# Kernel tuning notes

Hardware: AMD Instinct MI355X
Metric: run time of the kernel (lower is better)

Reference implementation:

```python
import jax, jax.numpy as jnp
import numpy as np

N, IN_CH, HID, HEADS, OUT_CH, E = 50000, 128, 64, 4, 16, 800000
NEG_SLOPE = 0.2


def gatv2_layer(x, Wl, Wr, att, b, src, dst, n_nodes, heads, out_ch, concat):
    # lin_l -> source features, lin_r -> target features (PyG GATv2Conv, share_weights=False)
    xl = (x @ Wl).reshape(n_nodes, heads, out_ch)
    xr = (x @ Wr).reshape(n_nodes, heads, out_ch)
    # per-edge attention logits: att . leaky_relu(x_l[j] + x_r[i])
    e = jax.nn.leaky_relu(xl[src] + xr[dst], NEG_SLOPE)        # [E, H, C]
    logits = jnp.einsum('ehc,hc->eh', e, att)                  # [E, H]
    # softmax over incoming edges per target node
    m = jax.ops.segment_max(logits, dst, num_segments=n_nodes)
    ex = jnp.exp(logits - m[dst])
    denom = jax.ops.segment_sum(ex, dst, num_segments=n_nodes)
    alpha = ex / denom[dst]                                    # [E, H]
    # scatter weighted source messages back to targets
    msg = alpha[:, :, None] * xl[src]                          # [E, H, C]
    out = jax.ops.segment_sum(msg, dst, num_segments=n_nodes)  # [N, H, C]
    out = out.reshape(n_nodes, heads * out_ch) if concat else out.mean(axis=1)
    return out + b


def setup_inputs() -> dict:
    key = jax.random.key(0)
    ks = jax.random.split(key, 10)
    x = jax.random.normal(ks[0], (N, IN_CH), dtype=jnp.float32)
    edge_index = jax.random.randint(ks[1], (2, E), 0, N, dtype=jnp.int64)
    s1 = 1.0 / np.sqrt(IN_CH)
    s2 = 1.0 / np.sqrt(HEADS * HID)
    return {
        'x': x,
        'edge_index': edge_index,
        'W1l': jax.random.normal(ks[2], (IN_CH, HEADS * HID), dtype=jnp.float32) * s1,
        'W1r': jax.random.normal(ks[3], (IN_CH, HEADS * HID), dtype=jnp.float32) * s1,
        'att1': jax.random.normal(ks[4], (HEADS, HID), dtype=jnp.float32) * (1.0 / np.sqrt(HID)),
        'b1': jnp.zeros((HEADS * HID,), dtype=jnp.float32),
        'W2l': jax.random.normal(ks[5], (HEADS * HID, OUT_CH), dtype=jnp.float32) * s2,
        'W2r': jax.random.normal(ks[6], (HEADS * HID, OUT_CH), dtype=jnp.float32) * s2,
        'att2': jax.random.normal(ks[7], (1, OUT_CH), dtype=jnp.float32) * (1.0 / np.sqrt(OUT_CH)),
        'b2': jnp.zeros((OUT_CH,), dtype=jnp.float32),
    }


def reference(x, edge_index, W1l, W1r, att1, b1, W2l, W2r, att2, b2):
    # add self loops (PyG GATv2Conv default add_self_loops=True)
    loops = jnp.arange(N, dtype=edge_index.dtype)
    src = jnp.concatenate([edge_index[0], loops])
    dst = jnp.concatenate([edge_index[1], loops])
    h = gatv2_layer(x, W1l, W1r, att1, b1, src, dst, N, HEADS, HID, True)
    h = jax.nn.elu(h)
    out = gatv2_layer(h, W2l, W2r, att2, b2, src, dst, N, 1, OUT_CH, False)
    return out
```

## Files before the change

kernel.cpp:

```cpp
#include <hip/hip_runtime.h>
#include <hip/hip_bf16.h>
#include <math.h>

#define N_NODES 50000
#define IN_CH   128
#define HID     64
#define HEADS   4
#define OUT_CH  16
#define NE      800000
#define ETOT    (NE + N_NODES)
#define NEG_SLOPE 0.2f

__global__ __launch_bounds__(256) void k_gemm1(const float* __restrict__ x,
        const float* __restrict__ Wl, const float* __restrict__ Wr,
        float* __restrict__ out) {
    __shared__ float xs[64][132];
    __shared__ float ws[128][64];
    int rb = blockIdx.x * 64;
    int cb = blockIdx.y * 64;
    const float* W = (cb < 256) ? Wl : Wr;
    int wc = cb & 255;
    int tid = threadIdx.x;
    for (int i = 0; i < 8; ++i) {
        int idx = i * 256 + tid;
        int r = idx >> 5, c4 = idx & 31;
        float4 v = make_float4(0.f, 0.f, 0.f, 0.f);
        int gr = rb + r;
        if (gr < N_NODES) v = *(const float4*)(x + (size_t)gr * IN_CH + c4 * 4);
        *(float4*)&xs[r][c4 * 4] = v;
    }
    for (int i = 0; i < 8; ++i) {
        int idx = i * 256 + tid;
        int r = idx >> 4, c4 = idx & 15;
        *(float4*)&ws[r][c4 * 4] = *(const float4*)(W + (size_t)r * 256 + wc + c4 * 4);
    }
    __syncthreads();
    int cg = tid & 15, rg = tid >> 4;
    int c0 = cg * 4, r0 = rg * 4;
    float acc[4][4];
    #pragma unroll
    for (int i = 0; i < 4; ++i)
        #pragma unroll
        for (int j = 0; j < 4; ++j) acc[i][j] = 0.f;
    for (int k = 0; k < 128; ++k) {
        float xv[4];
        #pragma unroll
        for (int i = 0; i < 4; ++i) xv[i] = xs[r0 + i][k];
        float4 wv = *(float4*)&ws[k][c0];
        #pragma unroll
        for (int i = 0; i < 4; ++i) {
            acc[i][0] += xv[i] * wv.x;
            acc[i][1] += xv[i] * wv.y;
            acc[i][2] += xv[i] * wv.z;
            acc[i][3] += xv[i] * wv.w;
        }
    }
    #pragma unroll
    for (int i = 0; i < 4; ++i) {
        int gr = rb + r0 + i;
        if (gr < N_NODES) {
            float4 v = make_float4(acc[i][0], acc[i][1], acc[i][2], acc[i][3]);
            *(float4*)(out + (size_t)gr * 512 + cb + c0) = v;
        }
    }
}

__global__ void k_count(const int* __restrict__ ei, int* __restrict__ counts) {
    int e = blockIdx.x * blockDim.x + threadIdx.x;
    if (e >= ETOT) return;
    int dst = (e < NE) ? ei[NE + e] : (e - NE);
    atomicAdd(&counts[dst], 1);
}

__global__ __launch_bounds__(256) void k_scanA(const int* __restrict__ counts,
        int* __restrict__ tmp, int* __restrict__ bsums) {
    __shared__ int lds[256];
    int i = blockIdx.x * 256 + threadIdx.x;
    int v = (i < N_NODES) ? counts[i] : 0;
    lds[threadIdx.x] = v;
    __syncthreads();
    int val = v;
    for (int off = 1; off < 256; off <<= 1) {
        int t = (threadIdx.x >= off) ? lds[threadIdx.x - off] : 0;
        __syncthreads();
        val += t;
        lds[threadIdx.x] = val;
        __syncthreads();
    }
    if (i < N_NODES) tmp[i] = val;
    if (threadIdx.x == 255) bsums[blockIdx.x] = val;
}

__global__ __launch_bounds__(256) void k_scanB(const int* __restrict__ bsums,
        int* __restrict__ boff, int nb) {
    __shared__ int lds[256];
    int tid = threadIdx.x;
    int v = (tid < nb) ? bsums[tid] : 0;
    lds[tid] = v;
    __syncthreads();
    int val = v;
    for (int off = 1; off < 256; off <<= 1) {
        int t = (tid >= off) ? lds[tid - off] : 0;
        __syncthreads();
        val += t;
        lds[tid] = val;
        __syncthreads();
    }
    if (tid < nb) boff[tid] = val - v;
}

__global__ void k_scanC(const int* __restrict__ tmp, const int* __restrict__ counts,
        const int* __restrict__ boff, int* __restrict__ rowptr, int* __restrict__ cursor) {
    int i = blockIdx.x * 256 + threadIdx.x;
    if (i >= N_NODES) return;
    int ex = tmp[i] + boff[blockIdx.x] - counts[i];
    rowptr[i] = ex;
    cursor[i] = ex;
    if (i == N_NODES - 1) rowptr[N_NODES] = ex + counts[i];
}

__global__ void k_fill(const int* __restrict__ ei, int* __restrict__ cursor,
        int* __restrict__ csrc) {
    int e = blockIdx.x * blockDim.x + threadIdx.x;
    if (e >= ETOT) return;
    int src, dst;
    if (e < NE) { src = ei[e]; dst = ei[NE + e]; }
    else        { src = e - NE; dst = src; }
    int pos = atomicAdd(&cursor[dst], 1);
    csrc[pos] = src;
}

__device__ __forceinline__ float edge_logit(float4 xl, float4 xr, float4 av) {
    float4 u;
    u.x = xl.x + xr.x; u.y = xl.y + xr.y; u.z = xl.z + xr.z; u.w = xl.w + xr.w;
    u.x = (u.x > 0.f) ? u.x : u.x * NEG_SLOPE;
    u.y = (u.y > 0.f) ? u.y : u.y * NEG_SLOPE;
    u.z = (u.z > 0.f) ? u.z : u.z * NEG_SLOPE;
    u.w = (u.w > 0.f) ? u.w : u.w * NEG_SLOPE;
    return u.x * av.x + u.y * av.y + u.z * av.z + u.w * av.w;
}

__global__ __launch_bounds__(256) void k_agg1(const float* __restrict__ xlxr,
        const int* __restrict__ rowptr, const int* __restrict__ csrc,
        const float* __restrict__ att, const float* __restrict__ b1,
        float* __restrict__ h) {
    int wave = threadIdx.x >> 6, lane = threadIdx.x & 63;
    int d = blockIdx.x * 4 + wave;
    if (d >= N_NODES) return;
    int hh = lane >> 4, cb = (lane & 15) * 4;
    int co = hh * 64 + cb;
    const float* base_l = xlxr + co;
    float4 xr = *(const float4*)(xlxr + (size_t)d * 512 + 256 + co);
    float4 av = *(const float4*)(att + co);
    float m = -1e30f, s = 0.f;
    float4 acc = make_float4(0.f, 0.f, 0.f, 0.f);
    int e0 = rowptr[d], e1 = rowptr[d + 1];
    int i = e0;
    for (; i + 1 < e1; i += 2) {
        int s0 = csrc[i], s1 = csrc[i + 1];
        float4 x0 = *(const float4*)(base_l + (size_t)s0 * 512);
        float4 x1 = *(const float4*)(base_l + (size_t)s1 * 512);
        float t0 = edge_logit(x0, xr, av);
        float t1 = edge_logit(x1, xr, av);
        t0 += __shfl_xor(t0, 8, 64);  t1 += __shfl_xor(t1, 8, 64);
        t0 += __shfl_xor(t0, 4, 64);  t1 += __shfl_xor(t1, 4, 64);
        t0 += __shfl_xor(t0, 2, 64);  t1 += __shfl_xor(t1, 2, 64);
        t0 += __shfl_xor(t0, 1, 64);  t1 += __shfl_xor(t1, 1, 64);
        {
            float nm = fmaxf(m, t0);
            float sc = __expf(m - nm), p = __expf(t0 - nm);
            s = s * sc + p;
            acc.x = acc.x * sc + p * x0.x;
            acc.y = acc.y * sc + p * x0.y;
            acc.z = acc.z * sc + p * x0.z;
            acc.w = acc.w * sc + p * x0.w;
            m = nm;
        }
        {
            float nm = fmaxf(m, t1);
            float sc = __expf(m - nm), p = __expf(t1 - nm);
            s = s * sc + p;
            acc.x = acc.x * sc + p * x1.x;
            acc.y = acc.y * sc + p * x1.y;
            acc.z = acc.z * sc + p * x1.z;
            acc.w = acc.w * sc + p * x1.w;
            m = nm;
        }
    }
    if (i < e1) {
        int s0 = csrc[i];
        float4 x0 = *(const float4*)(base_l + (size_t)s0 * 512);
        float t0 = edge_logit(x0, xr, av);
        t0 += __shfl_xor(t0, 8, 64);
        t0 += __shfl_xor(t0, 4, 64);
        t0 += __shfl_xor(t0, 2, 64);
        t0 += __shfl_xor(t0, 1, 64);
        float nm = fmaxf(m, t0);
        float sc = __expf(m - nm), p = __expf(t0 - nm);
        s = s * sc + p;
        acc.x = acc.x * sc + p * x0.x;
        acc.y = acc.y * sc + p * x0.y;
        acc.z = acc.z * sc + p * x0.z;
        acc.w = acc.w * sc + p * x0.w;
        m = nm;
    }
    float inv = 1.f / s;
    float4 bv = *(const float4*)(b1 + co);
    float4 v;
    v.x = acc.x * inv + bv.x;
    v.y = acc.y * inv + bv.y;
    v.z = acc.z * inv + bv.z;
    v.w = acc.w * inv + bv.w;
    v.x = (v.x > 0.f) ? v.x : (__expf(v.x) - 1.f);
    v.y = (v.y > 0.f) ? v.y : (__expf(v.y) - 1.f);
    v.z = (v.z > 0.f) ? v.z : (__expf(v.z) - 1.f);
    v.w = (v.w > 0.f) ? v.w : (__expf(v.w) - 1.f);
    *(float4*)(h + (size_t)d * 256 + co) = v;
}

__global__ __launch_bounds__(256) void k_gemm2(const float* __restrict__ h,
        const float* __restrict__ W2l, const float* __restrict__ W2r,
        float* __restrict__ out) {
    __shared__ float ws[256 * 32];
    int tid = threadIdx.x;
    for (int i = 0; i < 32; ++i) {
        int idx = i * 256 + tid;
        int k = idx >> 5, mm = idx & 31;
        ws[idx] = (mm < 16) ? W2l[k * 16 + mm] : W2r[k * 16 + (mm - 16)];
    }
    __syncthreads();
    int wave = tid >> 6, lane = tid & 63;
    int mm = lane & 31, kh = lane >> 5;
    for (int n = blockIdx.x * 4 + wave; n < N_NODES; n += gridDim.x * 4) {
        float acc = 0.f;
        const float* hp = h + (size_t)n * 256 + kh * 128;
        #pragma unroll
        for (int kk4 = 0; kk4 < 32; ++kk4) {
            float4 hv = *(const float4*)(hp + kk4 * 4);
            int kb = (kh * 128 + kk4 * 4) * 32 + mm;
            acc += hv.x * ws[kb] + hv.y * ws[kb + 32] + hv.z * ws[kb + 64] + hv.w * ws[kb + 96];
        }
        acc += __shfl_xor(acc, 32, 64);
        if (lane < 32) out[(size_t)n * 32 + mm] = acc;
    }
}

__global__ __launch_bounds__(256) void k_agg2(const float* __restrict__ xlxr2,
        const int* __restrict__ rowptr, const int* __restrict__ csrc,
        const float* __restrict__ att2, const float* __restrict__ b2,
        float* __restrict__ out) {
    int wave = threadIdx.x >> 6, lane = threadIdx.x & 63;
    int d = blockIdx.x * 4 + wave;
    if (d >= N_NODES) return;
    int g = lane >> 4, c = lane & 15;
    float xrv = xlxr2[(size_t)d * 32 + 16 + c];
    float a   = att2[c];
    float m = -1e30f, s = 0.f, acc = 0.f;
    int e0 = rowptr[d], e1 = rowptr[d + 1];
    for (int i = e0 + g; i < e1; i += 4) {
        int src = csrc[i];
        float xl = xlxr2[(size_t)src * 32 + c];
        float u = xl + xrv;
        u = (u > 0.f) ? u : u * NEG_SLOPE;
        float t = u * a;
        t += __shfl_xor(t, 8, 64);
        t += __shfl_xor(t, 4, 64);
        t += __shfl_xor(t, 2, 64);
        t += __shfl_xor(t, 1, 64);
        float nm = fmaxf(m, t);
        float sc = __expf(m - nm), p = __expf(t - nm);
        s = s * sc + p;
        acc = acc * sc + p * xl;
        m = nm;
    }
    #pragma unroll
    for (int off = 16; off <= 32; off <<= 1) {
        float mo = __shfl_xor(m, off, 64);
        float so = __shfl_xor(s, off, 64);
        float ao = __shfl_xor(acc, off, 64);
        float nm = fmaxf(m, mo);
        float ea = __expf(m - nm), eb = __expf(mo - nm);
        s   = s * ea + so * eb;
        acc = acc * ea + ao * eb;
        m = nm;
    }
    if (lane < 16) out[(size_t)d * 16 + c] = acc / s + b2[c];
}

extern "C" void kernel_launch(void* const* d_in, const int* in_sizes, int n_in,
                              void* d_out, int out_size, void* d_ws, size_t ws_size,
                              hipStream_t stream) {
    const float* x    = (const float*)d_in[0];
    const int*   ei   = (const int*)d_in[1];
    const float* W1l  = (const float*)d_in[2];
    const float* W1r  = (const float*)d_in[3];
    const float* att1 = (const float*)d_in[4];
    const float* b1   = (const float*)d_in[5];
    const float* W2l  = (const float*)d_in[6];
    const float* W2r  = (const float*)d_in[7];
    const float* att2 = (const float*)d_in[8];
    const float* b2   = (const float*)d_in[9];
    float* outp = (float*)d_out;

    char* wsb = (char*)d_ws;
    size_t off = 0;
    auto alloc = [&](size_t bytes) {
        void* p = wsb + off;
        off = (off + bytes + 255) & ~(size_t)255;
        return p;
    };
    float* xlxr1 = (float*)alloc((size_t)N_NODES * 512 * 4);
    float* h1    = (float*)alloc((size_t)N_NODES * 256 * 4);
    float* xlxr2 = (float*)alloc((size_t)N_NODES * 32 * 4);
    int* rowptr  = (int*)alloc((N_NODES + 1) * 4);
    int* cursor  = (int*)alloc(N_NODES * 4);
    int* counts  = (int*)alloc(N_NODES * 4);
    int* tmp     = (int*)alloc(N_NODES * 4);
    int* bsums   = (int*)alloc(256 * 4);
    int* boff    = (int*)alloc(256 * 4);
    int* csrc    = (int*)alloc((size_t)ETOT * 4);

    hipMemsetAsync(counts, 0, N_NODES * 4, stream);

    dim3 g1((N_NODES + 63) / 64, 8);
    k_gemm1<<<g1, 256, 0, stream>>>(x, W1l, W1r, xlxr1);

    int nb = (N_NODES + 255) / 256;
    k_count<<<(ETOT + 255) / 256, 256, 0, stream>>>(ei, counts);
    k_scanA<<<nb, 256, 0, stream>>>(counts, tmp, bsums);
    k_scanB<<<1, 256, 0, stream>>>(bsums, boff, nb);
    k_scanC<<<nb, 256, 0, stream>>>(tmp, counts, boff, rowptr, cursor);
    k_fill<<<(ETOT + 255) / 256, 256, 0, stream>>>(ei, cursor, csrc);

    k_agg1<<<(N_NODES + 3) / 4, 256, 0, stream>>>(xlxr1, rowptr, csrc, att1, b1, h1);
    k_gemm2<<<1280, 256, 0, stream>>>(h1, W2l, W2r, xlxr2);
    k_agg2<<<(N_NODES + 3) / 4, 256, 0, stream>>>(xlxr2, rowptr, csrc, att2, b2, outp);
}
```

Baseline: 499.5 us.

## Merge scan kernels, fold counts zeroing into GEMM, reuse x tile, unroll agg1

Three changes are combined. The counts memset moves into k_gemm1, and each GEMM block now loops over all 8 output column tiles, so the x tile is loaded into LDS once instead of eight times. The three-kernel prefix scan becomes a single 1024-thread block scan, which cuts launch count. k_agg1 now processes 4 edges per iteration instead of 2 to expose more memory-level parallelism. The tradeoffs are fewer GEMM blocks, less parallelism in the scan, and higher register pressure in agg1.

```diff
diff --git a/kernel.cpp b/kernel.cpp
--- a/kernel.cpp
+++ b/kernel.cpp
@@ -13,14 +13,14 @@
 
 __global__ __launch_bounds__(256) void k_gemm1(const float* __restrict__ x,
         const float* __restrict__ Wl, const float* __restrict__ Wr,
-        float* __restrict__ out) {
+        float* __restrict__ out, int* __restrict__ counts) {
+    int tid = threadIdx.x;
+    int zi = blockIdx.x * 256 + tid;
+    if (zi < N_NODES) counts[zi] = 0;
+
     __shared__ float xs[64][132];
     __shared__ float ws[128][64];
     int rb = blockIdx.x * 64;
-    int cb = blockIdx.y * 64;
-    const float* W = (cb < 256) ? Wl : Wr;
-    int wc = cb & 255;
-    int tid = threadIdx.x;
     for (int i = 0; i < 8; ++i) {
         int idx = i * 256 + tid;
         int r = idx >> 5, c4 = idx & 31;
@@ -29,38 +29,46 @@
         if (gr < N_NODES) v = *(const float4*)(x + (size_t)gr * IN_CH + c4 * 4);
         *(float4*)&xs[r][c4 * 4] = v;
     }
-    for (int i = 0; i < 8; ++i) {
-        int idx = i * 256 + tid;
-        int r = idx >> 4, c4 = idx & 15;
-        *(float4*)&ws[r][c4 * 4] = *(const float4*)(W + (size_t)r * 256 + wc + c4 * 4);
-    }
-    __syncthreads();
     int cg = tid & 15, rg = tid >> 4;
     int c0 = cg * 4, r0 = rg * 4;
-    float acc[4][4];
-    #pragma unroll
-    for (int i = 0; i < 4; ++i)
-        #pragma unroll
-        for (int j = 0; j < 4; ++j) acc[i][j] = 0.f;
-    for (int k = 0; k < 128; ++k) {
-        float xv[4];
-        #pragma unroll
-        for (int i = 0; i < 4; ++i) xv[i] = xs[r0 + i][k];
-        float4 wv = *(float4*)&ws[k][c0];
+
+    for (int ct = 0; ct < 8; ++ct) {
+        int cb = ct * 64;
+        const float* W = (ct < 4) ? Wl : Wr;
+        int wc = cb & 255;
+        __syncthreads();
+        for (int i = 0; i < 8; ++i) {
+            int idx = i * 256 + tid;
+            int r = idx >> 4, c4 = idx & 15;
+            *(float4*)&ws[r][c4 * 4] = *(const float4*)(W + (size_t)r * 256 + wc + c4 * 4);
+        }
+        __syncthreads();
+
+        float acc[4][4];
+        #pragma unroll
+        for (int i = 0; i < 4; ++i)
+            #pragma unroll
+            for (int j = 0; j < 4; ++j) acc[i][j] = 0.f;
+        for (int k = 0; k < 128; ++k) {
+            float xv[4];
+            #pragma unroll
+            for (int i = 0; i < 4; ++i) xv[i] = xs[r0 + i][k];
+            float4 wv = *(float4*)&ws[k][c0];
+            #pragma unroll
+            for (int i = 0; i < 4; ++i) {
+                acc[i][0] += xv[i] * wv.x;
+                acc[i][1] += xv[i] * wv.y;
+                acc[i][2] += xv[i] * wv.z;
+                acc[i][3] += xv[i] * wv.w;
+            }
+        }
         #pragma unroll
         for (int i = 0; i < 4; ++i) {
-            acc[i][0] += xv[i] * wv.x;
-            acc[i][1] += xv[i] * wv.y;
-            acc[i][2] += xv[i] * wv.z;
-            acc[i][3] += xv[i] * wv.w;
-        }
-    }
-    #pragma unroll
-    for (int i = 0; i < 4; ++i) {
-        int gr = rb + r0 + i;
-        if (gr < N_NODES) {
-            float4 v = make_float4(acc[i][0], acc[i][1], acc[i][2], acc[i][3]);
-            *(float4*)(out + (size_t)gr * 512 + cb + c0) = v;
+            int gr = rb + r0 + i;
+            if (gr < N_NODES) {
+                float4 v = make_float4(acc[i][0], acc[i][1], acc[i][2], acc[i][3]);
+                *(float4*)(out + (size_t)gr * 512 + cb + c0) = v;
+            }
         }
     }
 }
@@ -72,51 +80,33 @@
     atomicAdd(&counts[dst], 1);
 }
 
-__global__ __launch_bounds__(256) void k_scanA(const int* __restrict__ counts,
-        int* __restrict__ tmp, int* __restrict__ bsums) {
-    __shared__ int lds[256];
-    int i = blockIdx.x * 256 + threadIdx.x;
-    int v = (i < N_NODES) ? counts[i] : 0;
-    lds[threadIdx.x] = v;
+#define SCAN_T 1024
+__global__ __launch_bounds__(SCAN_T) void k_scan(const int* __restrict__ counts,
+        int* __restrict__ rowptr, int* __restrict__ cursor) {
+    __shared__ int lds[SCAN_T];
+    int t = threadIdx.x;
+    const int C = (N_NODES + SCAN_T - 1) / SCAN_T;
+    int b = t * C;
+    int e = b + C; if (e > N_NODES) e = N_NODES;
+    int sum = 0;
+    for (int i = b; i < e; ++i) sum += counts[i];
+    lds[t] = sum;
     __syncthreads();
-    int val = v;
-    for (int off = 1; off < 256; off <<= 1) {
-        int t = (threadIdx.x >= off) ? lds[threadIdx.x - off] : 0;
+    int val = sum;
+    for (int off = 1; off < SCAN_T; off <<= 1) {
+        int tv = (t >= off) ? lds[t - off] : 0;
         __syncthreads();
-        val += t;
-        lds[threadIdx.x] = val;
+        val += tv;
+        lds[t] = val;
         __syncthreads();
     }
-    if (i < N_NODES) tmp[i] = val;
-    if (threadIdx.x == 255) bsums[blockIdx.x] = val;
-}
-
-__global__ __launch_bounds__(256) void k_scanB(const int* __restrict__ bsums,
-        int* __restrict__ boff, int nb) {
-    __shared__ int lds[256];
-    int tid = threadIdx.x;
-    int v = (tid < nb) ? bsums[tid] : 0;
-    lds[tid] = v;
-    __syncthreads();
-    int val = v;
-    for (int off = 1; off < 256; off <<= 1) {
-        int t = (tid >= off) ? lds[tid - off] : 0;
-        __syncthreads();
-        val += t;
-        lds[tid] = val;
-        __syncthreads();
-    }
-    if (tid < nb) boff[tid] = val - v;
-}
-
-__global__ void k_scanC(const int* __restrict__ tmp, const int* __restrict__ counts,
-        const int* __restrict__ boff, int* __restrict__ rowptr, int* __restrict__ cursor) {
-    int i = blockIdx.x * 256 + threadIdx.x;
-    if (i >= N_NODES) return;
-    int ex = tmp[i] + boff[blockIdx.x] - counts[i];
-    rowptr[i] = ex;
-    cursor[i] = ex;
-    if (i == N_NODES - 1) rowptr[N_NODES] = ex + counts[i];
+    int run = val - sum;
+    for (int i = b; i < e; ++i) {
+        rowptr[i] = run;
+        cursor[i] = run;
+        run += counts[i];
+    }
+    if (b < N_NODES && e == N_NODES) rowptr[N_NODES] = run;
 }
 
 __global__ void k_fill(const int* __restrict__ ei, int* __restrict__ cursor,
@@ -138,6 +128,18 @@
     u.z = (u.z > 0.f) ? u.z : u.z * NEG_SLOPE;
     u.w = (u.w > 0.f) ? u.w : u.w * NEG_SLOPE;
     return u.x * av.x + u.y * av.y + u.z * av.z + u.w * av.w;
+}
+
+__device__ __forceinline__ void sm_update(float t, float4 xv,
+        float& m, float& s, float4& acc) {
+    float nm = fmaxf(m, t);
+    float sc = __expf(m - nm), p = __expf(t - nm);
+    s = s * sc + p;
+    acc.x = acc.x * sc + p * xv.x;
+    acc.y = acc.y * sc + p * xv.y;
+    acc.z = acc.z * sc + p * xv.z;
+    acc.w = acc.w * sc + p * xv.w;
+    m = nm;
 }
 
 __global__ __launch_bounds__(256) void k_agg1(const float* __restrict__ xlxr,
@@ -156,53 +158,35 @@
     float4 acc = make_float4(0.f, 0.f, 0.f, 0.f);
     int e0 = rowptr[d], e1 = rowptr[d + 1];
     int i = e0;
-    for (; i + 1 < e1; i += 2) {
-        int s0 = csrc[i], s1 = csrc[i + 1];
+    for (; i + 3 < e1; i += 4) {
+        int s0 = csrc[i], s1 = csrc[i + 1], s2 = csrc[i + 2], s3 = csrc[i + 3];
         float4 x0 = *(const float4*)(base_l + (size_t)s0 * 512);
         float4 x1 = *(const float4*)(base_l + (size_t)s1 * 512);
+        float4 x2 = *(const float4*)(base_l + (size_t)s2 * 512);
+        float4 x3 = *(const float4*)(base_l + (size_t)s3 * 512);
         float t0 = edge_logit(x0, xr, av);
         float t1 = edge_logit(x1, xr, av);
-        t0 += __shfl_xor(t0, 8, 64);  t1 += __shfl_xor(t1, 8, 64);
-        t0 += __shfl_xor(t0, 4, 64);  t1 += __shfl_xor(t1, 4, 64);
-        t0 += __shfl_xor(t0, 2, 64);  t1 += __shfl_xor(t1, 2, 64);
-        t0 += __shfl_xor(t0, 1, 64);  t1 += __shfl_xor(t1, 1, 64);
-        {
-            float nm = fmaxf(m, t0);
-            float sc = __expf(m - nm), p = __expf(t0 - nm);
-            s = s * sc + p;
-            acc.x = acc.x * sc + p * x0.x;
-            acc.y = acc.y * sc + p * x0.y;
-            acc.z = acc.z * sc + p * x0.z;
-            acc.w = acc.w * sc + p * x0.w;
-            m = nm;
-        }
-        {
-            float nm = fmaxf(m, t1);
-            float sc = __expf(m - nm), p = __expf(t1 - nm);
-            s = s * sc + p;
-            acc.x = acc.x * sc + p * x1.x;
-            acc.y = acc.y * sc + p * x1.y;
-            acc.z = acc.z * sc + p * x1.z;
-            acc.w = acc.w * sc + p * x1.w;
-            m = nm;
-        }
-    }
-    if (i < e1) {
+        float t2 = edge_logit(x2, xr, av);
+        float t3 = edge_logit(x3, xr, av);
+        #pragma unroll
+        for (int off = 8; off >= 1; off >>= 1) {
+            t0 += __shfl_xor(t0, off, 64);
+            t1 += __shfl_xor(t1, off, 64);
+            t2 += __shfl_xor(t2, off, 64);
+            t3 += __shfl_xor(t3, off, 64);
+        }
+        sm_update(t0, x0, m, s, acc);
+        sm_update(t1, x1, m, s, acc);
+        sm_update(t2, x2, m, s, acc);
+        sm_update(t3, x3, m, s, acc);
+    }
+    for (; i < e1; ++i) {
         int s0 = csrc[i];
         float4 x0 = *(const float4*)(base_l + (size_t)s0 * 512);
         float t0 = edge_logit(x0, xr, av);
-        t0 += __shfl_xor(t0, 8, 64);
-        t0 += __shfl_xor(t0, 4, 64);
-        t0 += __shfl_xor(t0, 2, 64);
-        t0 += __shfl_xor(t0, 1, 64);
-        float nm = fmaxf(m, t0);
-        float sc = __expf(m - nm), p = __expf(t0 - nm);
-        s = s * sc + p;
-        acc.x = acc.x * sc + p * x0.x;
-        acc.y = acc.y * sc + p * x0.y;
-        acc.z = acc.z * sc + p * x0.z;
-        acc.w = acc.w * sc + p * x0.w;
-        m = nm;
+        #pragma unroll
+        for (int off = 8; off >= 1; off >>= 1) t0 += __shfl_xor(t0, off, 64);
+        sm_update(t0, x0, m, s, acc);
     }
     float inv = 1.f / s;
     float4 bv = *(const float4*)(b1 + co);
@@ -315,21 +299,12 @@
     int* rowptr  = (int*)alloc((N_NODES + 1) * 4);
     int* cursor  = (int*)alloc(N_NODES * 4);
     int* counts  = (int*)alloc(N_NODES * 4);
-    int* tmp     = (int*)alloc(N_NODES * 4);
-    int* bsums   = (int*)alloc(256 * 4);
-    int* boff    = (int*)alloc(256 * 4);
     int* csrc    = (int*)alloc((size_t)ETOT * 4);
 
-    hipMemsetAsync(counts, 0, N_NODES * 4, stream);
-
-    dim3 g1((N_NODES + 63) / 64, 8);
-    k_gemm1<<<g1, 256, 0, stream>>>(x, W1l, W1r, xlxr1);
-
-    int nb = (N_NODES + 255) / 256;
+    k_gemm1<<<(N_NODES + 63) / 64, 256, 0, stream>>>(x, W1l, W1r, xlxr1, counts);
+
     k_count<<<(ETOT + 255) / 256, 256, 0, stream>>>(ei, counts);
-    k_scanA<<<nb, 256, 0, stream>>>(counts, tmp, bsums);
-    k_scanB<<<1, 256, 0, stream>>>(bsums, boff, nb);
-    k_scanC<<<nb, 256, 0, stream>>>(tmp, counts, boff, rowptr, cursor);
+    k_scan<<<1, SCAN_T, 0, stream>>>(counts, rowptr, cursor);
     k_fill<<<(ETOT + 255) / 256, 256, 0, stream>>>(ei, cursor, csrc);
 
     k_agg1<<<(N_NODES + 3) / 4, 256, 0, stream>>>(xlxr1, rowptr, csrc, att1, b1, h1);
```

Measured after the change: 611.0 us. 1.22x slower.
